# Performance work log

Hardware: AMD Instinct MI355X
Metric: run time of the kernel (lower is better)

The kernel has to match this reference:

```python
import jax, jax.numpy as jnp
import numpy as np

H, KV, D, HID = 16, 8, 128, 2048  # n_heads, n_kv_heads, head_dim, hidden_size
EPS = 1e-6
SCALE = D ** -0.5


def rotate_half(x):
    x1, x2 = x[..., : x.shape[-1] // 2], x[..., x.shape[-1] // 2 :]
    return jnp.concatenate((-x2, x1), axis=-1)


def rms_norm(x, w, eps=EPS):
    xf = x.astype(jnp.float32)
    xf = xf * jax.lax.rsqrt(jnp.mean(jnp.square(xf), axis=-1, keepdims=True) + eps)
    return (w * xf).astype(x.dtype)


def setup_inputs() -> dict:
    key = jax.random.key(0)
    ks = jax.random.split(key, 8)
    B, S = 2, 2048
    x = jax.random.normal(ks[0], (B, S, HID), dtype=jnp.float32)
    # RoPE tables from rope_theta frequencies
    theta = 5e6
    inv_freq = 1.0 / (theta ** (np.arange(0, D, 2, dtype=np.float32) / D))  # (D/2,)
    pos = np.arange(S, dtype=np.float32)
    freqs = np.outer(pos, inv_freq)  # (S, D/2)
    emb = np.concatenate([freqs, freqs], axis=-1)  # (S, D)
    sin = jnp.broadcast_to(jnp.asarray(np.sin(emb)), (B, S, D)).astype(jnp.float32)
    cos = jnp.broadcast_to(jnp.asarray(np.cos(emb)), (B, S, D)).astype(jnp.float32)
    # causal additive mask (B, 1, S, S)
    causal = jnp.where(jnp.tril(jnp.ones((S, S), dtype=bool)), 0.0, -1e9).astype(jnp.float32)
    attention_mask = jnp.broadcast_to(causal[None, None], (B, 1, S, S))
    std = 0.02
    Wq = jax.random.normal(ks[1], (HID, H * D), dtype=jnp.float32) * std
    Wk = jax.random.normal(ks[2], (HID, KV * D), dtype=jnp.float32) * std
    Wv = jax.random.normal(ks[3], (HID, KV * D), dtype=jnp.float32) * std
    Wo = jax.random.normal(ks[4], (H * D, HID), dtype=jnp.float32) * std
    q_norm_w = jnp.ones((D,), dtype=jnp.float32)
    k_norm_w = jnp.ones((D,), dtype=jnp.float32)
    return dict(x=x, sin=sin, cos=cos, attention_mask=attention_mask,
                Wq=Wq, Wk=Wk, Wv=Wv, Wo=Wo, q_norm_w=q_norm_w, k_norm_w=k_norm_w)


def reference(x, sin, cos, attention_mask, Wq, Wk, Wv, Wo, q_norm_w, k_norm_w):
    B, S, _ = x.shape
    groups = H // KV
    q = (x @ Wq).reshape(B, S, H, D)
    k = (x @ Wk).reshape(B, S, KV, D)
    v = (x @ Wv).reshape(B, S, KV, D)
    q = rms_norm(q, q_norm_w)
    k = rms_norm(k, k_norm_w)
    c, s = cos[:, :, None, :], sin[:, :, None, :]
    q = q * c + rotate_half(q) * s
    k = k * c + rotate_half(k) * s
    if groups > 1:
        k = jnp.repeat(k, groups, axis=2)  # (B,S,H,D)
        v = jnp.repeat(v, groups, axis=2)
    attn = jnp.einsum('bihd,bjhd->bhij', q, k) * SCALE  # (B,H,S,S)
    attn = jax.nn.softmax(attn + attention_mask, axis=-1)
    out = jnp.einsum('bhij,bjhd->bihd', attn, v).reshape(B, S, H * D)
    return out @ Wo
```

## Files before the change

### kernel.cpp

```cpp
#include <hip/hip_runtime.h>
#include <hip/hip_bf16.h>
#include <math.h>

#define H_    16
#define KV_   8
#define D_    128
#define HID_  2048
#define NQKV_ 4096
#define SCALE_ 0.08838834764831845f

typedef __attribute__((ext_vector_type(8))) short bf16x8;
typedef __attribute__((ext_vector_type(4))) float f32x4;
typedef __attribute__((ext_vector_type(4))) short short4v;

__device__ inline unsigned short f2bf(float f) {
  unsigned u = __builtin_bit_cast(unsigned, f);
  u += 0x7FFF + ((u >> 16) & 1);
  return (unsigned short)(u >> 16);
}

#define GLDS16(g, l)                                                     \
  __builtin_amdgcn_global_load_lds(                                      \
      (const __attribute__((address_space(1))) void*)(g),                \
      (__attribute__((address_space(3))) void*)(l), 16, 0, 0)

__global__ __launch_bounds__(256) void f32_to_bf16(
    const float* __restrict__ in, unsigned short* __restrict__ out, int n8) {
  int i = blockIdx.x * 256 + threadIdx.x;
  if (i >= n8) return;
  const float4* p = (const float4*)in + (size_t)i * 2;
  float4 a = p[0], b = p[1];
  unsigned short o[8] = {f2bf(a.x), f2bf(a.y), f2bf(a.z), f2bf(a.w),
                         f2bf(b.x), f2bf(b.y), f2bf(b.z), f2bf(b.w)};
  *(bf16x8*)(out + (size_t)i * 8) = *(bf16x8*)o;
}

__global__ __launch_bounds__(256) void transpose_bf16(
    const float* __restrict__ in, unsigned short* __restrict__ out, int K, int N) {
  __shared__ float t[32][33];
  const int k0 = blockIdx.y * 32, n0 = blockIdx.x * 32;
  const int r = threadIdx.x >> 3, c4 = (threadIdx.x & 7) * 4;
  float4 v = *(const float4*)(in + (size_t)(k0 + r) * N + n0 + c4);
  t[r][c4 + 0] = v.x; t[r][c4 + 1] = v.y; t[r][c4 + 2] = v.z; t[r][c4 + 3] = v.w;
  __syncthreads();
  unsigned short o[4];
#pragma unroll
  for (int j = 0; j < 4; ++j) o[j] = f2bf(t[c4 + j][r]);
  *(short4v*)(out + (size_t)(n0 + r) * K + k0 + c4) = *(short4v*)o;
}

__global__ __launch_bounds__(256) void transpose_qkv3(
    const float* __restrict__ Wq, const float* __restrict__ Wk,
    const float* __restrict__ Wv, unsigned short* __restrict__ out) {
  __shared__ float t[32][33];
  const int n0 = blockIdx.x * 32;
  const int k0 = blockIdx.y * 32;
  const float* src; int N, nloc;
  if (n0 < H_ * D_)                  { src = Wq; N = H_ * D_;  nloc = n0; }
  else if (n0 < H_ * D_ + KV_ * D_)  { src = Wk; N = KV_ * D_; nloc = n0 - H_ * D_; }
  else                               { src = Wv; N = KV_ * D_; nloc = n0 - H_ * D_ - KV_ * D_; }
  const int r = threadIdx.x >> 3, c4 = (threadIdx.x & 7) * 4;
  float4 v = *(const float4*)(src + (size_t)(k0 + r) * N + nloc + c4);
  t[r][c4 + 0] = v.x; t[r][c4 + 1] = v.y; t[r][c4 + 2] = v.z; t[r][c4 + 3] = v.w;
  __syncthreads();
  unsigned short o[4];
#pragma unroll
  for (int j = 0; j < 4; ++j) o[j] = f2bf(t[c4 + j][r]);
  *(short4v*)(out + (size_t)(n0 + r) * HID_ + k0 + c4) = *(short4v*)o;
}

#define TBM 128
#define TBN 128
#define TBK 64

template <int EPI>
__global__ __launch_bounds__(256) void gemm_bf16(
    const unsigned short* __restrict__ A,
    const unsigned short* __restrict__ Bt,
    float* __restrict__ C0, float* __restrict__ C1,
    unsigned short* __restrict__ C2, int M, int N, int K, int S) {
  __shared__ unsigned short As[TBM * TBK];
  __shared__ unsigned short Bs[TBN * TBK];
  const int tid = threadIdx.x;
  const int w = tid >> 6, lane = tid & 63;
  const int wm = w >> 1, wn = w & 1;
  const int fr = lane & 15, fq = lane >> 4;
  const int row0 = blockIdx.y * TBM, col0 = blockIdx.x * TBN;

  const unsigned short* Ab = A + (size_t)row0 * K;
  const unsigned short* Bb = Bt + (size_t)col0 * K;
  const int sm = lane >> 3;
  const int sk = (lane & 7) * 8;

  f32x4 acc[4][4] = {};

  for (int k0 = 0; k0 < K; k0 += TBK) {
    __syncthreads();
#pragma unroll
    for (int p = 0; p < 4; ++p) {
      const int seg = w * 4 + p;
      const int m = seg * 8 + sm;
      GLDS16(Ab + (size_t)m * K + k0 + sk, As + seg * 512);
      GLDS16(Bb + (size_t)m * K + k0 + sk, Bs + seg * 512);
    }
    __syncthreads();
#pragma unroll
    for (int s = 0; s < 2; ++s) {
      bf16x8 af[4], bfr[4];
#pragma unroll
      for (int i = 0; i < 4; ++i)
        af[i] = *(const bf16x8*)(As + (wm * 64 + i * 16 + fr) * TBK + s * 32 + fq * 8);
#pragma unroll
      for (int j = 0; j < 4; ++j)
        bfr[j] = *(const bf16x8*)(Bs + (wn * 64 + j * 16 + fr) * TBK + s * 32 + fq * 8);
#pragma unroll
      for (int i = 0; i < 4; ++i)
#pragma unroll
        for (int j = 0; j < 4; ++j)
          acc[i][j] = __builtin_amdgcn_mfma_f32_16x16x32_bf16(af[i], bfr[j], acc[i][j], 0, 0, 0);
    }
  }

  if constexpr (EPI == 0) {
#pragma unroll
    for (int i = 0; i < 4; ++i)
#pragma unroll
      for (int j = 0; j < 4; ++j) {
        const int col = col0 + wn * 64 + j * 16 + fr;
#pragma unroll
        for (int r = 0; r < 4; ++r) {
          const int row = row0 + wm * 64 + i * 16 + fq * 4 + r;
          C0[(size_t)row * N + col] = acc[i][j][r];
        }
      }
  } else {
    if (col0 < H_ * D_) {
#pragma unroll
      for (int i = 0; i < 4; ++i)
#pragma unroll
        for (int j = 0; j < 4; ++j) {
          const int col = col0 + wn * 64 + j * 16 + fr;
#pragma unroll
          for (int r = 0; r < 4; ++r) {
            const int row = row0 + wm * 64 + i * 16 + fq * 4 + r;
            C0[(size_t)row * (H_ * D_) + col] = acc[i][j][r];
          }
        }
    } else if (col0 < H_ * D_ + KV_ * D_) {
#pragma unroll
      for (int i = 0; i < 4; ++i)
#pragma unroll
        for (int j = 0; j < 4; ++j) {
          const int col = col0 - H_ * D_ + wn * 64 + j * 16 + fr;
#pragma unroll
          for (int r = 0; r < 4; ++r) {
            const int row = row0 + wm * 64 + i * 16 + fq * 4 + r;
            C1[(size_t)row * (KV_ * D_) + col] = acc[i][j][r];
          }
        }
    } else {
#pragma unroll
      for (int i = 0; i < 4; ++i)
#pragma unroll
        for (int j = 0; j < 4; ++j) {
          const int cc = col0 - (H_ * D_ + KV_ * D_) + wn * 64 + j * 16 + fr;
          const int kvh = cc >> 7, d = cc & 127;
          const int row = row0 + wm * 64 + i * 16 + fq * 4;
          const int b = row / S, s = row - b * S;
          unsigned short o[4] = {f2bf(acc[i][j][0]), f2bf(acc[i][j][1]),
                                 f2bf(acc[i][j][2]), f2bf(acc[i][j][3])};
          *(short4v*)(C2 + ((size_t)(b * KV_ + kvh) * D_ + d) * S + s) = *(short4v*)o;
        }
    }
  }
}

__global__ __launch_bounds__(256) void rmsnorm_rope_o16(
    const float* __restrict__ p, unsigned short* __restrict__ o16,
    const float* __restrict__ w, const float* __restrict__ cs,
    const float* __restrict__ sn, int nheads, float oscale) {
  const int row  = blockIdx.x * 4 + (threadIdx.x >> 6);
  const int lane = threadIdx.x & 63;
  const float* base = p + (size_t)row * D_;
  float x1 = base[lane];
  float x2 = base[lane + 64];
  float ss = x1 * x1 + x2 * x2;
#pragma unroll
  for (int m = 32; m; m >>= 1) ss += __shfl_xor(ss, m);
  float r = rsqrtf(ss * (1.0f / 128.0f) + 1e-6f);
  const size_t sidx = (size_t)(row / nheads) * D_;
  float n1 = x1 * r * w[lane];
  float n2 = x2 * r * w[lane + 64];
  unsigned short* ob = o16 + (size_t)row * D_;
  ob[lane]      = f2bf((n1 * cs[sidx + lane]      - n2 * sn[sidx + lane])      * oscale);
  ob[lane + 64] = f2bf((n2 * cs[sidx + lane + 64] + n1 * sn[sidx + lane + 64]) * oscale);
}

__global__ __launch_bounds__(256) void flash_bf16(
    const unsigned short* __restrict__ Qb, const unsigned short* __restrict__ Kb,
    const unsigned short* __restrict__ Vt, unsigned short* __restrict__ O,
    int S, int nqt) {
  __shared__ unsigned short Kt[128 * 128];
  __shared__ unsigned short Vs[128 * 128];
  __shared__ unsigned short Pl[4][16 * 128];
  const int h = blockIdx.y, b = blockIdx.z;
  const int kvh = h >> 1;
  const int tid = threadIdx.x, w = tid >> 6, lane = tid & 63;
  const int fr = lane & 15, fq = lane >> 4;
  const int rl = lane >> 4;
  const int sch = lane & 15;
  const unsigned short* vhead = Vt + (size_t)(b * KV_ + kvh) * D_ * S;

#pragma unroll 1
  for (int half = 0; half < 2; ++half) {
    const int qt = half ? (nqt - 1 - (int)blockIdx.x) : (int)blockIdx.x;
    const int q0 = qt * 64;
    const int nkt = (q0 + 64 + 127) >> 7;

    bf16x8 qf[4];
    {
      const unsigned short* qp =
          Qb + ((size_t)(b * S + q0 + w * 16 + fr) * H_ + h) * D_;
#pragma unroll
      for (int s = 0; s < 4; ++s) qf[s] = *(const bf16x8*)(qp + s * 32 + fq * 8);
    }

    f32x4 acco[8] = {};
    float mrow[4] = {-1e30f, -1e30f, -1e30f, -1e30f};
    float lrow[4] = {0.f, 0.f, 0.f, 0.f};

#pragma unroll 1
    for (int kt = 0; kt < nkt; ++kt) {
      __syncthreads();
#pragma unroll
      for (int p = 0; p < 8; ++p) {
        const int r = p * 16 + w * 4 + rl;
        const int gch = (sch & 8) | ((sch ^ r) & 7);
        GLDS16(Kb + ((size_t)(b * S + kt * 128 + r) * KV_ + kvh) * D_ + gch * 8,
               Kt + (p * 16 + w * 4) * 128);
        GLDS16(vhead + (size_t)r * S + kt * 128 + gch * 8,
               Vs + (p * 16 + w * 4) * 128);
      }
      __syncthreads();

      f32x4 sa[8];
      __builtin_amdgcn_s_setprio(1);
#pragma unroll
      for (int t = 0; t < 8; ++t) {
        f32x4 a = {};
        const int kv = 16 * t + fr;
#pragma unroll
        for (int s = 0; s < 4; ++s) {
          const int ch = 4 * s + fq;
          const int chs = (ch & 8) | ((ch ^ kv) & 7);
          bf16x8 kf = *(const bf16x8*)(Kt + kv * 128 + chs * 8);
          a = __builtin_amdgcn_mfma_f32_16x16x32_bf16(qf[s], kf, a, 0, 0, 0);
        }
        sa[t] = a;
      }
      __builtin_amdgcn_s_setprio(0);

      if (kt == nkt - 1) {
#pragma unroll
        for (int t = 0; t < 8; ++t) {
          const int kvg = kt * 128 + 16 * t + fr;
#pragma unroll
          for (int r = 0; r < 4; ++r)
            if (kvg > q0 + w * 16 + fq * 4 + r) sa[t][r] = -1e30f;
        }
      }

      float al[4];
#pragma unroll
      for (int r = 0; r < 4; ++r) {
        float mx = sa[0][r];
#pragma unroll
        for (int t = 1; t < 8; ++t) mx = fmaxf(mx, sa[t][r]);
        mx = fmaxf(mx, __shfl_xor(mx, 1));
        mx = fmaxf(mx, __shfl_xor(mx, 2));
        mx = fmaxf(mx, __shfl_xor(mx, 4));
        mx = fmaxf(mx, __shfl_xor(mx, 8));
        const float mn = fmaxf(mrow[r], mx);
        al[r] = __expf(mrow[r] - mn);
        mrow[r] = mn;
        float sum = 0.f;
#pragma unroll
        for (int t = 0; t < 8; ++t) {
          const float pv = __expf(sa[t][r] - mn);
          sa[t][r] = pv;
          sum += pv;
        }
        sum += __shfl_xor(sum, 1);
        sum += __shfl_xor(sum, 2);
        sum += __shfl_xor(sum, 4);
        sum += __shfl_xor(sum, 8);
        lrow[r] = lrow[r] * al[r] + sum;
#pragma unroll
        for (int c = 0; c < 8; ++c) acco[c][r] *= al[r];
      }

      unsigned short* pw = &Pl[w][0];
#pragma unroll
      for (int t = 0; t < 8; ++t) {
        const int kv = 16 * t + fr;
        const int ch = kv >> 3;
#pragma unroll
        for (int r = 0; r < 4; ++r) {
          const int q = fq * 4 + r;
          pw[q * 128 + ((ch & 8) | ((ch ^ q) & 7)) * 8 + (kv & 7)] = f2bf(sa[t][r]);
        }
      }

      bf16x8 pf[4];
#pragma unroll
      for (int s = 0; s < 4; ++s) {
        const int ch = 4 * s + fq;
        pf[s] = *(const bf16x8*)(pw + fr * 128 + ((ch & 8) | ((ch ^ fr) & 7)) * 8);
      }
      __builtin_amdgcn_s_setprio(1);
#pragma unroll
      for (int c = 0; c < 8; ++c) {
        const int d = 16 * c + fr;
#pragma unroll
        for (int s = 0; s < 4; ++s) {
          const int ch = 4 * s + fq;
          bf16x8 vf = *(const bf16x8*)(Vs + d * 128 + ((ch & 8) | ((ch ^ d) & 7)) * 8);
          acco[c] = __builtin_amdgcn_mfma_f32_16x16x32_bf16(pf[s], vf, acco[c], 0, 0, 0);
        }
      }
      __builtin_amdgcn_s_setprio(0);
    }

    float inv[4];
#pragma unroll
    for (int r = 0; r < 4; ++r) inv[r] = 1.0f / lrow[r];
#pragma unroll
    for (int c = 0; c < 8; ++c) {
#pragma unroll
      for (int r = 0; r < 4; ++r) {
        const int q = q0 + w * 16 + fq * 4 + r;
        O[(size_t)(b * S + q) * (H_ * D_) + h * D_ + 16 * c + fr] =
            f2bf(acco[c][r] * inv[r]);
      }
    }
  }
}

extern "C" void kernel_launch(void* const* d_in, const int* in_sizes, int n_in,
                              void* d_out, int out_size, void* d_ws, size_t ws_size,
                              hipStream_t stream) {
  const float* x  = (const float*)d_in[0];
  const float* sn = (const float*)d_in[1];
  const float* cs = (const float*)d_in[2];
  const float* Wq = (const float*)d_in[4];
  const float* Wk = (const float*)d_in[5];
  const float* Wv = (const float*)d_in[6];
  const float* Wo = (const float*)d_in[7];
  const float* qw = (const float*)d_in[8];
  const float* kw = (const float*)d_in[9];
  float* out = (float*)d_out;

  const int BS = in_sizes[0] / HID_;
  const int S  = in_sizes[3] / BS;
  const int B  = BS / S;

  float* kbuf = (float*)d_ws;
  unsigned short* vt   = (unsigned short*)(kbuf + (size_t)BS * KV_ * D_);
  unsigned short* xb   = vt + (size_t)BS * KV_ * D_;
  unsigned short* wT   = xb + (size_t)BS * HID_;
  unsigned short* qb   = wT + (size_t)NQKV_ * HID_;
  unsigned short* kb16 = qb + (size_t)BS * H_ * D_;
  unsigned short* ab16 = xb;

  dim3 blk(256);
  const int n8x = BS * HID_ / 8;

  f32_to_bf16<<<dim3(n8x / 256), blk, 0, stream>>>(x, xb, n8x);

  transpose_qkv3<<<dim3(NQKV_ / 32, HID_ / 32), blk, 0, stream>>>(Wq, Wk, Wv, wT);

  gemm_bf16<1><<<dim3(NQKV_ / TBN, BS / TBM), blk, 0, stream>>>(
      xb, wT, out, kbuf, vt, BS, NQKV_, HID_, S);

  rmsnorm_rope_o16<<<dim3(BS * H_ / 4),  blk, 0, stream>>>(out,  qb,   qw, cs, sn, H_,  SCALE_);
  rmsnorm_rope_o16<<<dim3(BS * KV_ / 4), blk, 0, stream>>>(kbuf, kb16, kw, cs, sn, KV_, 1.0f);

  flash_bf16<<<dim3(S / 128, H_, B), blk, 0, stream>>>(qb, kb16, vt, ab16, S, S / 64);

  transpose_bf16<<<dim3(HID_ / 32, (H_ * D_) / 32), blk, 0, stream>>>(Wo, wT, H_ * D_, HID_);
  gemm_bf16<0><<<dim3(HID_ / TBN, BS / TBM), blk, 0, stream>>>(
      ab16, wT, out, nullptr, nullptr, BS, HID_, HID_, S);
}
```

Baseline: 403.8 us.

## Replace GEMM with 256x256 double-buffered, LDS-swizzled 512-thread kernel

Replaces the 128x128 single-buffered bf16 GEMM used for the QKV and output projections with a 256x256 tile, 512-thread kernel. Global-to-LDS loads are double-buffered with explicit vmcnt waits and barriers so the next K tile loads while MFMAs run. LDS columns are XOR-swizzled to reduce bank conflicts, and setprio raises wave priority around the MFMA section. The larger tiles give fewer blocks: 16x16=256 for QKV and 8x16=128 for the output projection, which may underfill 256 CUs. LDS use also grows to 128KB per block, which limits occupancy.

```diff
diff --git a/kernel.cpp b/kernel.cpp
--- a/kernel.cpp
+++ b/kernel.cpp
@@ -69,103 +69,132 @@
   *(short4v*)(out + (size_t)(n0 + r) * HID_ + k0 + c4) = *(short4v*)o;
 }
 
-#define TBM 128
-#define TBN 128
-#define TBK 64
+#define QBM 256
+#define QBN 256
+#define QBK 64
 
 template <int EPI>
-__global__ __launch_bounds__(256) void gemm_bf16(
+__global__ __launch_bounds__(512, 2) void gemm256(
     const unsigned short* __restrict__ A,
     const unsigned short* __restrict__ Bt,
     float* __restrict__ C0, float* __restrict__ C1,
     unsigned short* __restrict__ C2, int M, int N, int K, int S) {
-  __shared__ unsigned short As[TBM * TBK];
-  __shared__ unsigned short Bs[TBN * TBK];
+  __shared__ unsigned short As[2][QBM * QBK];
+  __shared__ unsigned short Bs[2][QBN * QBK];
   const int tid = threadIdx.x;
   const int w = tid >> 6, lane = tid & 63;
-  const int wm = w >> 1, wn = w & 1;
+  const int wm = w >> 2, wn = w & 3;
   const int fr = lane & 15, fq = lane >> 4;
-  const int row0 = blockIdx.y * TBM, col0 = blockIdx.x * TBN;
+  const int row0 = blockIdx.y * QBM, col0 = blockIdx.x * QBN;
 
   const unsigned short* Ab = A + (size_t)row0 * K;
   const unsigned short* Bb = Bt + (size_t)col0 * K;
-  const int sm = lane >> 3;
-  const int sk = (lane & 7) * 8;
-
-  f32x4 acc[4][4] = {};
-
-  for (int k0 = 0; k0 < K; k0 += TBK) {
-    __syncthreads();
-#pragma unroll
-    for (int p = 0; p < 4; ++p) {
-      const int seg = w * 4 + p;
-      const int m = seg * 8 + sm;
-      GLDS16(Ab + (size_t)m * K + k0 + sk, As + seg * 512);
-      GLDS16(Bb + (size_t)m * K + k0 + sk, Bs + seg * 512);
-    }
-    __syncthreads();
+  const int srow = w * 8 + (lane >> 3);
+  const int sc   = lane & 7;
+  const int nt   = K / QBK;
+
+  f32x4 acc[8][4] = {};
+
+#define STAGE256(t_, buf_)                                                      \
+  {                                                                             \
+    const int k0_ = (t_) * QBK;                                                 \
+    _Pragma("unroll")                                                           \
+    for (int p = 0; p < 4; ++p) {                                               \
+      const int r_ = p * 64 + srow;                                             \
+      const int gc_ = sc ^ (r_ & 7);                                            \
+      GLDS16(Ab + (size_t)r_ * K + k0_ + gc_ * 8,                               \
+             &As[buf_][(p * 64 + w * 8) * QBK]);                                \
+      GLDS16(Bb + (size_t)r_ * K + k0_ + gc_ * 8,                               \
+             &Bs[buf_][(p * 64 + w * 8) * QBK]);                                \
+    }                                                                           \
+  }
+
+  STAGE256(0, 0);
+  STAGE256(1, 1);
+  asm volatile("s_waitcnt vmcnt(8)" ::: "memory");
+  __builtin_amdgcn_s_barrier();
+  __builtin_amdgcn_sched_barrier(0);
+
+  for (int t = 0; t < nt; ++t) {
+    const int buf = t & 1;
+    __builtin_amdgcn_s_setprio(1);
 #pragma unroll
     for (int s = 0; s < 2; ++s) {
-      bf16x8 af[4], bfr[4];
-#pragma unroll
-      for (int i = 0; i < 4; ++i)
-        af[i] = *(const bf16x8*)(As + (wm * 64 + i * 16 + fr) * TBK + s * 32 + fq * 8);
-#pragma unroll
-      for (int j = 0; j < 4; ++j)
-        bfr[j] = *(const bf16x8*)(Bs + (wn * 64 + j * 16 + fr) * TBK + s * 32 + fq * 8);
-#pragma unroll
-      for (int i = 0; i < 4; ++i)
+      bf16x8 af[8], bf[4];
+#pragma unroll
+      for (int i = 0; i < 8; ++i) {
+        const int r = wm * 128 + i * 16 + fr;
+        af[i] = *(const bf16x8*)(&As[buf][r * QBK + (((s << 2) | fq) ^ (r & 7)) * 8]);
+      }
+#pragma unroll
+      for (int j = 0; j < 4; ++j) {
+        const int r = wn * 64 + j * 16 + fr;
+        bf[j] = *(const bf16x8*)(&Bs[buf][r * QBK + (((s << 2) | fq) ^ (r & 7)) * 8]);
+      }
+#pragma unroll
+      for (int i = 0; i < 8; ++i)
 #pragma unroll
         for (int j = 0; j < 4; ++j)
-          acc[i][j] = __builtin_amdgcn_mfma_f32_16x16x32_bf16(af[i], bfr[j], acc[i][j], 0, 0, 0);
-    }
+          acc[i][j] = __builtin_amdgcn_mfma_f32_16x16x32_bf16(af[i], bf[j], acc[i][j], 0, 0, 0);
+    }
+    __builtin_amdgcn_s_setprio(0);
+    __builtin_amdgcn_sched_barrier(0);
+    __builtin_amdgcn_s_barrier();
+    if (t + 2 < nt) {
+      STAGE256(t + 2, buf);
+      asm volatile("s_waitcnt vmcnt(8)" ::: "memory");
+    } else {
+      asm volatile("s_waitcnt vmcnt(0)" ::: "memory");
+    }
+    __builtin_amdgcn_s_barrier();
+    __builtin_amdgcn_sched_barrier(0);
   }
 
   if constexpr (EPI == 0) {
 #pragma unroll
-    for (int i = 0; i < 4; ++i)
+    for (int i = 0; i < 8; ++i)
 #pragma unroll
       for (int j = 0; j < 4; ++j) {
         const int col = col0 + wn * 64 + j * 16 + fr;
 #pragma unroll
         for (int r = 0; r < 4; ++r) {
-          const int row = row0 + wm * 64 + i * 16 + fq * 4 + r;
+          const int row = row0 + wm * 128 + i * 16 + fq * 4 + r;
           C0[(size_t)row * N + col] = acc[i][j][r];
         }
       }
   } else {
     if (col0 < H_ * D_) {
 #pragma unroll
-      for (int i = 0; i < 4; ++i)
+      for (int i = 0; i < 8; ++i)
 #pragma unroll
         for (int j = 0; j < 4; ++j) {
           const int col = col0 + wn * 64 + j * 16 + fr;
 #pragma unroll
           for (int r = 0; r < 4; ++r) {
-            const int row = row0 + wm * 64 + i * 16 + fq * 4 + r;
+            const int row = row0 + wm * 128 + i * 16 + fq * 4 + r;
             C0[(size_t)row * (H_ * D_) + col] = acc[i][j][r];
           }
         }
     } else if (col0 < H_ * D_ + KV_ * D_) {
 #pragma unroll
-      for (int i = 0; i < 4; ++i)
+      for (int i = 0; i < 8; ++i)
 #pragma unroll
         for (int j = 0; j < 4; ++j) {
           const int col = col0 - H_ * D_ + wn * 64 + j * 16 + fr;
 #pragma unroll
           for (int r = 0; r < 4; ++r) {
-            const int row = row0 + wm * 64 + i * 16 + fq * 4 + r;
+            const int row = row0 + wm * 128 + i * 16 + fq * 4 + r;
             C1[(size_t)row * (KV_ * D_) + col] = acc[i][j][r];
           }
         }
     } else {
 #pragma unroll
-      for (int i = 0; i < 4; ++i)
+      for (int i = 0; i < 8; ++i)
 #pragma unroll
         for (int j = 0; j < 4; ++j) {
           const int cc = col0 - (H_ * D_ + KV_ * D_) + wn * 64 + j * 16 + fr;
           const int kvh = cc >> 7, d = cc & 127;
-          const int row = row0 + wm * 64 + i * 16 + fq * 4;
+          const int row = row0 + wm * 128 + i * 16 + fq * 4;
           const int b = row / S, s = row - b * S;
           unsigned short o[4] = {f2bf(acc[i][j][0]), f2bf(acc[i][j][1]),
                                  f2bf(acc[i][j][2]), f2bf(acc[i][j][3])};
@@ -173,6 +202,7 @@
         }
     }
   }
+#undef STAGE256
 }
 
 __global__ __launch_bounds__(256) void rmsnorm_rope_o16(
@@ -379,7 +409,7 @@
 
   transpose_qkv3<<<dim3(NQKV_ / 32, HID_ / 32), blk, 0, stream>>>(Wq, Wk, Wv, wT);
 
-  gemm_bf16<1><<<dim3(NQKV_ / TBN, BS / TBM), blk, 0, stream>>>(
+  gemm256<1><<<dim3(NQKV_ / QBN, BS / QBM), dim3(512), 0, stream>>>(
       xb, wT, out, kbuf, vt, BS, NQKV_, HID_, S);
 
   rmsnorm_rope_o16<<<dim3(BS * H_ / 4),  blk, 0, stream>>>(out,  qb,   qw, cs, sn, H_,  SCALE_);
@@ -388,6 +418,6 @@
   flash_bf16<<<dim3(S / 128, H_, B), blk, 0, stream>>>(qb, kb16, vt, ab16, S, S / 64);
 
   transpose_bf16<<<dim3(HID_ / 32, (H_ * D_) / 32), blk, 0, stream>>>(Wo, wT, H_ * D_, HID_);
-  gemm_bf16<0><<<dim3(HID_ / TBN, BS / TBM), blk, 0, stream>>>(
+  gemm256<0><<<dim3(HID_ / QBN, BS / QBM), dim3(512), 0, stream>>>(
       ab16, wT, out, nullptr, nullptr, BS, HID_, HID_, S);
 }
```

After: 398.9 us. About the same (-1.2%).
